# Kernel tuning notes

Measured on AMD Instinct MI355X. Metric: run time of the kernel, lower is better.

Reference implementation:

```python
import jax, jax.numpy as jnp
import numpy as np
from jax import lax

N = 1024          # n_ligand == n_receptor == feature dim (required by broadcast in source)
D = 1024          # gnn_input_dim == gnn_output_dim
H = 32            # hopi_output_dim
C = 32            # cnn_channels


def setup_inputs() -> dict:
    key = jax.random.key(0)
    ks = jax.random.split(key, 24)
    s = 0.02
    inp = {
        "ligand_node_features": jax.random.normal(ks[0], (N, D), jnp.float32),
        "ligand_edge_features": jax.random.normal(ks[1], (N, D), jnp.float32),
        "ligand_adjacency": jax.random.uniform(ks[2], (N, N), jnp.float32),
        "receptor_node_features": jax.random.normal(ks[3], (N, D), jnp.float32),
        "receptor_edge_features": jax.random.normal(ks[4], (N, D), jnp.float32),
        "receptor_adjacency": jax.random.uniform(ks[5], (N, N), jnp.float32),
        # GNNLayer params (shared between ligand and receptor, as in source)
        "Wn": jax.random.normal(ks[6], (D, D), jnp.float32) * s,
        "bn": jax.random.normal(ks[7], (D,), jnp.float32) * s,
        "We": jax.random.normal(ks[8], (D, D), jnp.float32) * s,
        "be": jax.random.normal(ks[9], (D,), jnp.float32) * s,
        "Wa": jax.random.normal(ks[10], (1, D), jnp.float32) * s,
        "ba": jax.random.normal(ks[11], (1,), jnp.float32) * s,
        # HighOrderPairwiseInteraction: Linear(2*D -> H)
        "W_hopi": jax.random.normal(ks[12], (H, 2 * D), jnp.float32) * s,
        "b_hopi": jax.random.normal(ks[13], (H,), jnp.float32) * s,
        # CNN tail
        "conv1_w": jax.random.normal(ks[14], (C, H, 3, 3), jnp.float32) * s,
        "conv1_b": jax.random.normal(ks[15], (C,), jnp.float32) * s,
        "conv2_w": jax.random.normal(ks[16], (C, C, 3, 3), jnp.float32) * s,
        "conv2_b": jax.random.normal(ks[17], (C,), jnp.float32) * s,
        "conv3_w": jax.random.normal(ks[18], (1, C, 1, 1), jnp.float32) * s,
        "conv3_b": jax.random.normal(ks[19], (1,), jnp.float32) * s,
    }
    return inp


def _gnn(nf, ef, Wn, bn, We, be, Wa, ba):
    # aggregated: [N, D]
    agg = jnp.tanh(nf @ Wn.T + bn + ef @ We.T + be)
    scores = agg @ Wa.T + ba                      # [N, 1]
    attn = jax.nn.softmax(scores, axis=1)         # softmax over size-1 dim -> ones (faithful)
    weighted = jnp.sum(agg * attn, axis=1)        # [N]
    return nf + weighted                          # [N,D] + [N] broadcasts over last dim (D == N)


def _conv(x, w, b):
    y = lax.conv_general_dilated(x, w, (1, 1), "SAME",
                                 dimension_numbers=("NCHW", "OIHW", "NCHW"))
    return y + b[None, :, None, None]


def reference(ligand_node_features, ligand_edge_features, ligand_adjacency,
              receptor_node_features, receptor_edge_features, receptor_adjacency,
              Wn, bn, We, be, Wa, ba, W_hopi, b_hopi,
              conv1_w, conv1_b, conv2_w, conv2_b, conv3_w, conv3_b):
    lig = _gnn(ligand_node_features, ligand_edge_features, Wn, bn, We, be, Wa, ba)
    rec = _gnn(receptor_node_features, receptor_edge_features, Wn, bn, We, be, Wa, ba)

    # HOPI: interactions[i, j] = Linear(cat(lig[i], rec[j])) == lig[i] @ Wl.T + rec[j] @ Wr.T + b
    Wl, Wr = W_hopi[:, :D], W_hopi[:, D:]
    lig_p = lig @ Wl.T                            # [N, H]
    rec_p = rec @ Wr.T                            # [N, H]
    interactions = lig_p[:, None, :] + rec_p[None, :, :] + b_hopi  # [N, N, H]

    x = jnp.transpose(interactions, (2, 0, 1))[None]  # [1, H, N, N]
    x = jax.nn.relu(_conv(x, conv1_w, conv1_b))
    x = jax.nn.relu(_conv(x, conv2_w, conv2_b))
    x = _conv(x, conv3_w, conv3_b)                # [1, 1, N, N]
    return x[0, 0]                                # [N, N]
```

## Files before the change

### kernel.cpp

```cpp
#include <hip/hip_runtime.h>


typedef _Float16 half8 __attribute__((ext_vector_type(8)));
typedef _Float16 half4 __attribute__((ext_vector_type(4)));
typedef float    f32x4 __attribute__((ext_vector_type(4)));

__device__ __forceinline__ short f2h_bits(float f){
    _Float16 h = (_Float16)f;
    return __builtin_bit_cast(short, h);
}
__device__ __forceinline__ half8 pack2(const float4& x, const float4& y){
    half8 r;
    r[0] = (_Float16)x.x; r[1] = (_Float16)x.y;
    r[2] = (_Float16)x.z; r[3] = (_Float16)x.w;
    r[4] = (_Float16)y.x; r[5] = (_Float16)y.y;
    r[6] = (_Float16)y.z; r[7] = (_Float16)y.w;
    return r;
}
__device__ __forceinline__ half4 pack4(const float4& x){
    half4 r;
    r[0] = (_Float16)x.x; r[1] = (_Float16)x.y;
    r[2] = (_Float16)x.z; r[3] = (_Float16)x.w;
    return r;
}
__device__ __forceinline__ float tanh_fast(float x){
    float e = __expf(2.f * x);
    return 1.f - 2.f / (e + 1.f);
}

#define SWZ(c) ((((c) >> 1) & 3) << 3)

#define GNN_LOAD(AV, BV, KBN) {                                              \
    const int kbn_ = (KBN) & 2047;                                           \
    const float* Asrc_ = (kbn_ < 1024) ? A0 : A1;                            \
    const float* Bsrc_ = (kbn_ < 1024) ? Wn : We;                            \
    const int kk_ = kbn_ & 1023;                                             \
    const float* ap_ = Asrc_ + (size_t)(j0 + arow) * 1024 + kk_ + akc;       \
    const float* bp_ = Bsrc_ + (size_t)(d0 + brow) * 1024 + kk_ + bkc;       \
    AV[0] = *reinterpret_cast<const float4*>(ap_);                           \
    AV[1] = *reinterpret_cast<const float4*>(ap_ + 4);                       \
    AV[2] = *reinterpret_cast<const float4*>(ap_ + 8);                       \
    AV[3] = *reinterpret_cast<const float4*>(ap_ + 12);                      \
    BV[0] = *reinterpret_cast<const float4*>(bp_);                           \
    BV[1] = *reinterpret_cast<const float4*>(bp_ + 4);                       \
}

#define GNN_STAGE(AV, BV) {                                                  \
    const int ga_ = (t & 3) * 2;                                             \
    const int sa_ = arow & 7;                                                \
    *reinterpret_cast<half8*>(&As[arow * 64 + ((ga_    ) ^ sa_) * 8]) = pack2(AV[0], AV[1]); \
    *reinterpret_cast<half8*>(&As[arow * 64 + ((ga_ + 1) ^ sa_) * 8]) = pack2(AV[2], AV[3]); \
    *reinterpret_cast<half8*>(&Bs[brow * 64 + ((t & 7) ^ (brow & 7)) * 8]) = pack2(BV[0], BV[1]); \
}

#define GNN_MFMA() {                                                         \
    _Pragma("unroll")                                                        \
    for (int ks = 0; ks < 2; ++ks){                                          \
        half8 Af[2], Bf[2];                                                  \
        _Pragma("unroll")                                                    \
        for (int m = 0; m < 2; ++m){                                         \
            int row = wm * 32 + m * 16 + lr;                                 \
            int g   = ((ks * 4 + lg) ^ (row & 7)) * 8;                       \
            Af[m] = *reinterpret_cast<const half8*>(&As[row * 64 + g]);      \
        }                                                                    \
        _Pragma("unroll")                                                    \
        for (int n = 0; n < 2; ++n){                                         \
            int col = wn * 32 + n * 16 + lr;                                 \
            int g   = ((ks * 4 + lg) ^ (col & 7)) * 8;                       \
            Bf[n] = *reinterpret_cast<const half8*>(&Bs[col * 64 + g]);      \
        }                                                                    \
        _Pragma("unroll")                                                    \
        for (int m = 0; m < 2; ++m)                                          \
            _Pragma("unroll")                                                \
            for (int n = 0; n < 2; ++n)                                      \
                acc[m][n] = __builtin_amdgcn_mfma_f32_16x16x32_f16(          \
                    Af[m], Bf[n], acc[m][n], 0, 0, 0);                       \
    }                                                                        \
}

__global__ __launch_bounds__(512) void gnn_kernel(
    const float* __restrict__ lig_nf, const float* __restrict__ lig_ef,
    const float* __restrict__ rec_nf, const float* __restrict__ rec_ef,
    const float* __restrict__ Wn, const float* __restrict__ We,
    const float* __restrict__ bn, const float* __restrict__ be,
    float* __restrict__ part)
{
    __shared__ __attribute__((aligned(16))) short As[128 * 64];
    __shared__ __attribute__((aligned(16))) short Bs[64 * 64];
    __shared__ float red[128][2];

    const int t  = threadIdx.x;
    const int cx = blockIdx.z;
    const float* A0 = cx ? rec_nf : lig_nf;
    const float* A1 = cx ? rec_ef : lig_ef;
    const int j0 = blockIdx.x * 128;
    const int d0 = blockIdx.y * 64;

    const int wid  = t >> 6;
    const int wm   = wid >> 1;
    const int wn   = wid & 1;
    const int lane = t & 63;
    const int lr   = lane & 15;
    const int lg   = lane >> 4;

    f32x4 acc[2][2];
    #pragma unroll
    for (int m = 0; m < 2; ++m)
        #pragma unroll
        for (int n = 0; n < 2; ++n)
            acc[m][n] = (f32x4){0.f, 0.f, 0.f, 0.f};

    const int arow = t >> 2;
    const int akc  = (t & 3) * 16;
    const int brow = t >> 3;
    const int bkc  = (t & 7) * 8;

    float4 avA[4], bvA[2], avB[4], bvB[2];
    GNN_LOAD(avA, bvA, 0);
    GNN_LOAD(avB, bvB, 64);

    for (int kb = 0; kb < 2048; kb += 128){
        __syncthreads();
        GNN_STAGE(avA, bvA);
        GNN_LOAD(avA, bvA, kb + 128);
        __syncthreads();
        GNN_MFMA();
        __syncthreads();
        GNN_STAGE(avB, bvB);
        GNN_LOAD(avB, bvB, kb + 192);
        __syncthreads();
        GNN_MFMA();
    }

    float rowsum[2][4];
    #pragma unroll
    for (int m = 0; m < 2; ++m)
        #pragma unroll
        for (int jj = 0; jj < 4; ++jj) rowsum[m][jj] = 0.f;
    #pragma unroll
    for (int n = 0; n < 2; ++n){
        int d = d0 + wn * 32 + n * 16 + lr;
        float bias = bn[d] + be[d];
        #pragma unroll
        for (int m = 0; m < 2; ++m)
            #pragma unroll
            for (int jj = 0; jj < 4; ++jj)
                rowsum[m][jj] += tanh_fast(acc[m][n][jj] + bias);
    }
    #pragma unroll
    for (int mask = 1; mask < 16; mask <<= 1)
        #pragma unroll
        for (int m = 0; m < 2; ++m)
            #pragma unroll
            for (int jj = 0; jj < 4; ++jj)
                rowsum[m][jj] += __shfl_xor(rowsum[m][jj], mask);
    __syncthreads();
    if (lr == 0){
        #pragma unroll
        for (int m = 0; m < 2; ++m)
            #pragma unroll
            for (int jj = 0; jj < 4; ++jj)
                red[wm * 32 + m * 16 + lg * 4 + jj][wn] = rowsum[m][jj];
    }
    __syncthreads();
    if (t < 128)
        part[(size_t)cx * 16384 + (size_t)blockIdx.y * 1024 + j0 + t]
            = red[t][0] + red[t][1];
}

#define PP_LOAD(AV, BV, KBN) {                                               \
    const int kcol_ = (KBN) & 1023;                                          \
    _Pragma("unroll")                                                        \
    for (int p = 0; p < 3; ++p){                                             \
        int e_ = t + 512 * p;                                                \
        if (e_ < 1280){                                                      \
            int rowl_ = e_ >> 4;                                             \
            int grow_ = r0 - 8 + rowl_;                                      \
            if ((unsigned)grow_ < 1024u)                                     \
                AV[p] = *reinterpret_cast<const float4*>(                    \
                    nf + (size_t)grow_ * 1024 + kcol_ + (e_ & 15) * 4);      \
            else                                                             \
                AV[p] = make_float4(0.f, 0.f, 0.f, 0.f);                     \
        }                                                                    \
    }                                                                        \
    BV = *reinterpret_cast<const float4*>(                                   \
        W + (size_t)(t >> 4) * 2048 + kcol_ + (t & 15) * 4);                 \
}

#define PP_STAGE(AV, BV) {                                                   \
    _Pragma("unroll")                                                        \
    for (int p = 0; p < 3; ++p){                                             \
        int e_ = t + 512 * p;                                                \
        if (e_ < 1280){                                                      \
            int rowl_ = e_ >> 4;                                             \
            int ga_ = (e_ & 15) >> 1;                                        \
            int sub_ = (e_ & 1) * 4;                                         \
            *reinterpret_cast<half4*>(                                       \
                &As[rowl_ * 64 + ((ga_ ^ (rowl_ & 7)) * 8) + sub_]) = pack4(AV[p]); \
        }                                                                    \
    }                                                                        \
    {                                                                        \
        int row_ = t >> 4;                                                   \
        int ga_ = (t & 15) >> 1;                                             \
        int sub_ = (t & 1) * 4;                                              \
        *reinterpret_cast<half4*>(                                           \
            &Bs[row_ * 64 + ((ga_ ^ (row_ & 7)) * 8) + sub_]) = pack4(BV);   \
    }                                                                        \
}

#define PP_MFMA() {                                                          \
    if (wid < 5){                                                            \
        _Pragma("unroll")                                                    \
        for (int ks = 0; ks < 2; ++ks){                                      \
            int ar_ = wid * 16 + lr;                                         \
            half8 Af = *reinterpret_cast<const half8*>(                      \
                &As[ar_ * 64 + ((ks * 4 + lg) ^ (ar_ & 7)) * 8]);            \
            _Pragma("unroll")                                                \
            for (int n = 0; n < 2; ++n){                                     \
                int col_ = n * 16 + lr;                                      \
                half8 Bf = *reinterpret_cast<const half8*>(                  \
                    &Bs[col_ * 64 + ((ks * 4 + lg) ^ (col_ & 7)) * 8]);      \
                pacc[n] = __builtin_amdgcn_mfma_f32_16x16x32_f16(            \
                    Af, Bf, pacc[n], 0, 0, 0);                               \
            }                                                                \
        }                                                                    \
    }                                                                        \
}

__global__ __launch_bounds__(512) void pp_kernel(
    const float* __restrict__ lig_nf, const float* __restrict__ rec_nf,
    const float* __restrict__ W_hopi, const float* __restrict__ b_hopi,
    const float* __restrict__ w1, const float* __restrict__ b1,
    const float* __restrict__ w2,
    const float* __restrict__ part,
    float* __restrict__ Kp, short* __restrict__ U16, short* __restrict__ V16,
    short* __restrict__ w2f16)
{
    __shared__ __attribute__((aligned(16))) char smem[47232];
    const int t = threadIdx.x;
    const int role = blockIdx.x;

    if (role < 32){
        short* As = reinterpret_cast<short*>(smem);
        short* Bs = reinterpret_cast<short*>(smem + 10240);
        short* Pz = reinterpret_cast<short*>(smem + 14336);
        short* Ws = reinterpret_cast<short*>(smem + 20736);

        const int cx = role >> 4;
        const int r0 = (role & 15) * 64;
        const float* nf = cx ? rec_nf : lig_nf;
        const float* W  = W_hopi + (cx ? 1024 : 0);
        short* O = cx ? V16 : U16;

        const int wid = t >> 6;
        const int lane = t & 63;
        const int lr = lane & 15;
        const int lg = lane >> 4;

        for (int e = t; e < 9216; e += 512){
            int cs  = e / 3072;
            int rem = e - cs * 3072;
            int co  = rem / 96;
            int k   = rem - co * 96;
            int d   = k >> 5;
            int ci  = k & 31;
            int o_lo = (cs == 1) ? 1 : 0;
            int o_hi = (cs == 2) ? 1 : 2;
            float s = 0.f;
            for (int o = o_lo; o <= o_hi; ++o){
                int tap = cx ? (o * 3 + d) : (d * 3 + o);
                s += w1[co * 288 + ci * 9 + tap];
            }
            Ws[(cs * 32 + co) * 104 + k] = f2h_bits(s);
        }

        f32x4 pacc[2];
        pacc[0] = (f32x4){0.f, 0.f, 0.f, 0.f};
        pacc[1] = (f32x4){0.f, 0.f, 0.f, 0.f};

        float4 avA[3], avB[3];
        float4 bvA, bvB;
        PP_LOAD(avA, bvA, 0);
        PP_LOAD(avB, bvB, 64);

        for (int kb = 0; kb < 1024; kb += 128){
            __syncthreads();
            PP_STAGE(avA, bvA);
            PP_LOAD(avA, bvA, kb + 128);
            __syncthreads();
            PP_MFMA();
            __syncthreads();
            PP_STAGE(avB, bvB);
            PP_LOAD(avB, bvB, kb + 192);
            __syncthreads();
            PP_MFMA();
        }

        if (wid < 5){
            #pragma unroll
            for (int n = 0; n < 2; ++n)
                #pragma unroll
                for (int jj = 0; jj < 4; ++jj){
                    int rowl = wid * 16 + lg * 4 + jj;
                    Pz[rowl * 40 + n * 16 + lr] = f2h_bits(pacc[n][jj]);
                }
        }
        __syncthreads();

        if (wid < 4){
            f32x4 uacc[3][2];
            #pragma unroll
            for (int cs = 0; cs < 3; ++cs)
                #pragma unroll
                for (int n = 0; n < 2; ++n)
                    uacc[cs][n] = (f32x4){0.f, 0.f, 0.f, 0.f};
            #pragma unroll
            for (int d = 0; d < 3; ++d){
                int ar = wid * 16 + lr;
                half8 Ap = *reinterpret_cast<const half8*>(
                    &Pz[(7 + ar + d) * 40 + lg * 8]);
                #pragma unroll
                for (int cs = 0; cs < 3; ++cs)
                    #pragma unroll
                    for (int n = 0; n < 2; ++n){
                        half8 Bp = *reinterpret_cast<const half8*>(
                            &Ws[(cs * 32 + n * 16 + lr) * 104 + d * 32 + lg * 8]);
                        uacc[cs][n] = __builtin_amdgcn_mfma_f32_16x16x32_f16(
                            Ap, Bp, uacc[cs][n], 0, 0, 0);
                    }
            }
            #pragma unroll
            for (int cs = 0; cs < 3; ++cs)
                #pragma unroll
                for (int n = 0; n < 2; ++n)
                    #pragma unroll
                    for (int jj = 0; jj < 4; ++jj){
                        int grow = r0 + wid * 16 + lg * 4 + jj;
                        O[((size_t)(cs << 10) + grow) * 32 + n * 16 + lr]
                            = f2h_bits(uacc[cs][n][jj]);
                    }
        }
        return;
    }

    if (role == 33){
        for (int e = t; e < 9216; e += 512){
            int co  = e / 288;
            int rem = e - co * 288;
            int ci  = rem / 9;
            int tap = rem - ci * 9;
            w2f16[(tap * 32 + co) * 32 + (ci ^ SWZ(co))] = f2h_bits(w2[e]);
        }
        return;
    }

    float* ws_l = reinterpret_cast<float*>(smem);
    float* ws_r = reinterpret_cast<float*>(smem + 4096);
    float* red  = reinterpret_cast<float*>(smem + 8192);
    float* cvs  = reinterpret_cast<float*>(smem + 10240);
    float* w1s  = reinterpret_cast<float*>(smem + 10368);

    #pragma unroll
    for (int q = 0; q < 5; ++q){
        int i4 = t + q * 512;
        if (i4 < 2304)
            *reinterpret_cast<float4*>(&w1s[i4 * 4]) =
                *reinterpret_cast<const float4*>(w1 + i4 * 4);
    }
    for (int j = t; j < 1024; j += 512){
        float sl = 0.f, sr = 0.f;
        #pragma unroll
        for (int b = 0; b < 16; ++b){
            sl += part[b * 1024 + j];
            sr += part[16384 + b * 1024 + j];
        }
        ws_l[j] = sl; ws_r[j] = sr;
    }
    __syncthreads();
    {
        const int h = t & 31;
        const int seg = t >> 5;
        const float* wl = W_hopi + (size_t)h * 2048 + seg * 64;
        const float* wr = wl + 1024;
        float s = 0.f;
        #pragma unroll 8
        for (int j = 0; j < 64; j += 4){
            float4 a = *reinterpret_cast<const float4*>(wl + j);
            float4 b = *reinterpret_cast<const float4*>(wr + j);
            const float* l = &ws_l[seg * 64 + j];
            const float* r = &ws_r[seg * 64 + j];
            s = fmaf(l[0], a.x, s); s = fmaf(l[1], a.y, s);
            s = fmaf(l[2], a.z, s); s = fmaf(l[3], a.w, s);
            s = fmaf(r[0], b.x, s); s = fmaf(r[1], b.y, s);
            s = fmaf(r[2], b.z, s); s = fmaf(r[3], b.w, s);
        }
        red[t] = s;
    }
    __syncthreads();
    if (t < 32){
        float tot = b_hopi[t];
        #pragma unroll
        for (int g = 0; g < 16; ++g) tot += red[g * 32 + t];
        cvs[t] = tot;
    }
    __syncthreads();
    for (int e = t; e < 288; e += 512){
        int co  = e & 31;
        int cse = e >> 5;
        int yc  = cse / 3, xc = cse - yc * 3;
        float sum = b1[co];
        for (int ci = 0; ci < 32; ++ci){
            const float* wp = &w1s[co * 288 + ci * 9];
            float t00 = wp[0], t01 = wp[1], t02 = wp[2];
            float t10 = wp[3], t11 = wp[4], t12 = wp[5];
            float t20 = wp[6], t21 = wp[7], t22 = wp[8];
            float r0, r1, r2;
            if (xc == 0){ r0 = t00+t01+t02; r1 = t10+t11+t12; r2 = t20+t21+t22; }
            else if (xc == 1){ r0 = t01+t02; r1 = t11+t12; r2 = t21+t22; }
            else { r0 = t00+t01; r1 = t10+t11; r2 = t20+t21; }
            float wsum = (yc == 0) ? (r0+r1+r2) : ((yc == 1) ? (r1+r2) : (r0+r1));
            sum = fmaf(cvs[ci], wsum, sum);
        }
        Kp[cse * 32 + co] = sum;
    }
}

__global__ __launch_bounds__(512) void conv_kernel(
    const short* __restrict__ U16, const short* __restrict__ V16,
    const float* __restrict__ Kp, const short* __restrict__ w2f16,
    const float* __restrict__ b2,
    const float* __restrict__ w3, const float* __restrict__ b3,
    float* __restrict__ outp)
{
    __shared__ __attribute__((aligned(16))) short ys[18 * 18 * 32];
    __shared__ __attribute__((aligned(16))) short wB[9 * 32 * 32];

    const int t    = threadIdx.x;
    const int oy0  = blockIdx.y * 16;
    const int ox0  = blockIdx.x * 16;
    const int wid  = t >> 6;
    const int lane = t & 63;
    const int lr   = lane & 15;
    const int lg   = lane >> 4;

    {
        const uint4* src = reinterpret_cast<const uint4*>(w2f16);
        uint4* dst = reinterpret_cast<uint4*>(wB);
        #pragma unroll
        for (int e = t; e < 1152; e += 512)
            dst[e] = src[e];
    }
    const bool interior = (blockIdx.x >= 1) & (blockIdx.x <= 62) &
                          (blockIdx.y >= 1) & (blockIdx.y <= 62);
    if (interior){
        const int cp = (t & 7) * 4;
        half4 k00;
        {
            float4 kf = *reinterpret_cast<const float4*>(&Kp[cp]);
            k00[0] = (_Float16)kf.x; k00[1] = (_Float16)kf.y;
            k00[2] = (_Float16)kf.z; k00[3] = (_Float16)kf.w;
        }
        #pragma unroll
        for (int pass = 0; pass < 6; ++pass){
            int idx = t + pass * 512;
            if (idx < 2592){
                int po  = idx >> 3;
                int ryo = po / 18;
                int rxo = po - ryo * 18;
                int gy = oy0 - 1 + ryo, gx = ox0 - 1 + rxo;
                half4 u = *reinterpret_cast<const half4*>(&U16[gy * 32 + cp]);
                half4 v = *reinterpret_cast<const half4*>(&V16[gx * 32 + cp]);
                half4 r = u + v + k00;
                #pragma unroll
                for (int e = 0; e < 4; ++e)
                    r[e] = r[e] > (_Float16)0.f ? r[e] : (_Float16)0.f;
                *reinterpret_cast<half4*>(&ys[po * 32 + (cp ^ SWZ(rxo))]) = r;
            }
        }
    } else {
        #pragma unroll
        for (int pass = 0; pass < 6; ++pass){
            int idx = t + pass * 512;
            if (idx < 2592){
                int po  = idx >> 3;
                int cp  = (idx & 7) * 4;
                int ryo = po / 18;
                int rxo = po - ryo * 18;
                int gy = oy0 - 1 + ryo, gx = ox0 - 1 + rxo;
                half4 h = {(_Float16)0.f, (_Float16)0.f, (_Float16)0.f, (_Float16)0.f};
                if ((unsigned)gy < 1024u && (unsigned)gx < 1024u){
                    int yc = (gy == 0) ? 1 : ((gy == 1023) ? 2 : 0);
                    int xc = (gx == 0) ? 1 : ((gx == 1023) ? 2 : 0);
                    half4 u = *reinterpret_cast<const half4*>(
                        &U16[((size_t)(xc << 10) + gy) * 32 + cp]);
                    half4 v = *reinterpret_cast<const half4*>(
                        &V16[((size_t)(yc << 10) + gx) * 32 + cp]);
                    float4 k = *reinterpret_cast<const float4*>(&Kp[(yc * 3 + xc) * 32 + cp]);
                    h[0] = (_Float16)fmaxf((float)u[0] + (float)v[0] + k.x, 0.f);
                    h[1] = (_Float16)fmaxf((float)u[1] + (float)v[1] + k.y, 0.f);
                    h[2] = (_Float16)fmaxf((float)u[2] + (float)v[2] + k.z, 0.f);
                    h[3] = (_Float16)fmaxf((float)u[3] + (float)v[3] + k.w, 0.f);
                }
                *reinterpret_cast<half4*>(&ys[po * 32 + (cp ^ SWZ(rxo))]) = h;
            }
        }
    }
    __syncthreads();

    {
        half8 Bf[2][9];
        float bias[2], w3v[2];
        #pragma unroll
        for (int n = 0; n < 2; ++n){
            int co = n * 16 + lr;
            bias[n] = b2[co];
            w3v[n]  = w3[co];
            #pragma unroll
            for (int tap = 0; tap < 9; ++tap)
                Bf[n][tap] = *reinterpret_cast<const half8*>(
                    &wB[(tap * 32 + co) * 32 + ((lg * 8) ^ SWZ(co))]);
        }
        const float b3v = b3[0];
        for (int s = wid; s < 16; s += 8){
            int p  = s * 16 + lr;
            int ry = p >> 4;
            int rx = p & 15;
            f32x4 acc0 = {0.f, 0.f, 0.f, 0.f};
            f32x4 acc1 = {0.f, 0.f, 0.f, 0.f};
            #pragma unroll
            for (int tap = 0; tap < 9; ++tap){
                const int dy = tap / 3, dx = tap - (tap / 3) * 3;
                int pix = (ry + dy) * 18 + rx + dx;
                half8 A = *reinterpret_cast<const half8*>(
                    &ys[pix * 32 + ((lg * 8) ^ SWZ(rx + dx))]);
                acc0 = __builtin_amdgcn_mfma_f32_16x16x32_f16(A, Bf[0][tap], acc0, 0, 0, 0);
                acc1 = __builtin_amdgcn_mfma_f32_16x16x32_f16(A, Bf[1][tap], acc1, 0, 0, 0);
            }
            float part[4];
            #pragma unroll
            for (int j = 0; j < 4; ++j)
                part[j] = w3v[0] * fmaxf(acc0[j] + bias[0], 0.f)
                        + w3v[1] * fmaxf(acc1[j] + bias[1], 0.f);
            #pragma unroll
            for (int m = 1; m < 16; m <<= 1)
                #pragma unroll
                for (int j = 0; j < 4; ++j)
                    part[j] += __shfl_xor(part[j], m);
            if (lr == 0){
                float4 o = make_float4(part[0] + b3v, part[1] + b3v,
                                       part[2] + b3v, part[3] + b3v);
                *reinterpret_cast<float4*>(outp + (size_t)(oy0 + s) * 1024 + ox0 + lg * 4) = o;
            }
        }
    }
}

extern "C" void kernel_launch(void* const* d_in, const int* in_sizes, int n_in,
                              void* d_out, int out_size, void* d_ws, size_t ws_size,
                              hipStream_t stream)
{
    const float* lig_nf = (const float*)d_in[0];
    const float* lig_ef = (const float*)d_in[1];
    const float* rec_nf = (const float*)d_in[3];
    const float* rec_ef = (const float*)d_in[4];
    const float* Wn     = (const float*)d_in[6];
    const float* bn     = (const float*)d_in[7];
    const float* We     = (const float*)d_in[8];
    const float* be     = (const float*)d_in[9];
    const float* W_hopi = (const float*)d_in[12];
    const float* b_hopi = (const float*)d_in[13];
    const float* w1     = (const float*)d_in[14];
    const float* b1     = (const float*)d_in[15];
    const float* w2     = (const float*)d_in[16];
    const float* b2     = (const float*)d_in[17];
    const float* w3     = (const float*)d_in[18];
    const float* b3     = (const float*)d_in[19];
    float* outp = (float*)d_out;

    float* part  = (float*)d_ws;
    float* Kp    = (float*)((char*)d_ws + 393216);
    short* U16   = (short*)((char*)d_ws + 394368);
    short* V16   = (short*)((char*)d_ws + 590976);
    short* w2f16 = (short*)((char*)d_ws + 787584);

    dim3 g1(8, 16, 2);
    gnn_kernel<<<g1, 512, 0, stream>>>(lig_nf, lig_ef, rec_nf, rec_ef,
                                       Wn, We, bn, be, part);
    pp_kernel<<<34, 512, 0, stream>>>(lig_nf, rec_nf, W_hopi, b_hopi,
                                      w1, b1, w2, part, Kp, U16, V16, w2f16);
    dim3 g3(64, 64);
    conv_kernel<<<g3, 512, 0, stream>>>(U16, V16, Kp, w2f16, b2, w3, b3, outp);
}
```

Baseline: 114.9 us.

## Make conv blocks persistent over 8 tiles with double-buffered LDS and prefetch

The conv kernel now launches 512 blocks, each handling 8 horizontally adjacent 16x16 output tiles. The U rows and the conv2 weight fragments are loaded once and reused across those tiles, and the next tile's V values are prefetched into registers while MFMA work runs on a double-buffered LDS tile. The build also uses 8-wide half vectors instead of 4-wide, and the weight-prep loops in pp_kernel are unrolled. This cuts the per-block setup cost and the global loads, at the price of fewer concurrent blocks (512 on 256 CUs), more LDS and more registers per block.

```diff
diff --git a/kernel.cpp b/kernel.cpp
--- a/kernel.cpp
+++ b/kernel.cpp
@@ -257,7 +257,9 @@
         const int lr = lane & 15;
         const int lg = lane >> 4;
 
-        for (int e = t; e < 9216; e += 512){
+        #pragma unroll
+        for (int q = 0; q < 18; ++q){
+            int e = t + q * 512;
             int cs  = e / 3072;
             int rem = e - cs * 3072;
             int co  = rem / 96;
@@ -344,7 +346,9 @@
     }
 
     if (role == 33){
-        for (int e = t; e < 9216; e += 512){
+        #pragma unroll
+        for (int q = 0; q < 18; ++q){
+            int e = t + q * 512;
             int co  = e / 288;
             int rem = e - co * 288;
             int ci  = rem / 9;
@@ -432,17 +436,20 @@
     const float* __restrict__ w3, const float* __restrict__ b3,
     float* __restrict__ outp)
 {
-    __shared__ __attribute__((aligned(16))) short ys[18 * 18 * 32];
+    __shared__ __attribute__((aligned(16))) short ysbuf[2][18 * 18 * 32];
     __shared__ __attribute__((aligned(16))) short wB[9 * 32 * 32];
 
     const int t    = threadIdx.x;
-    const int oy0  = blockIdx.y * 16;
-    const int ox0  = blockIdx.x * 16;
     const int wid  = t >> 6;
     const int lane = t & 63;
     const int lr   = lane & 15;
     const int lg   = lane >> 4;
 
+    const int ty  = blockIdx.x >> 3;
+    const int oy0 = ty * 16;
+    const int tx0 = (blockIdx.x & 7) * 8;
+    const bool rowInt = (ty >= 1) && (ty <= 62);
+
     {
         const uint4* src = reinterpret_cast<const uint4*>(w2f16);
         uint4* dst = reinterpret_cast<uint4*>(wB);
@@ -450,81 +457,114 @@
         for (int e = t; e < 1152; e += 512)
             dst[e] = src[e];
     }
-    const bool interior = (blockIdx.x >= 1) & (blockIdx.x <= 62) &
-                          (blockIdx.y >= 1) & (blockIdx.y <= 62);
-    if (interior){
-        const int cp = (t & 7) * 4;
-        half4 k00;
-        {
-            float4 kf = *reinterpret_cast<const float4*>(&Kp[cp]);
-            k00[0] = (_Float16)kf.x; k00[1] = (_Float16)kf.y;
-            k00[2] = (_Float16)kf.z; k00[3] = (_Float16)kf.w;
-        }
-        #pragma unroll
-        for (int pass = 0; pass < 6; ++pass){
-            int idx = t + pass * 512;
-            if (idx < 2592){
-                int po  = idx >> 3;
-                int ryo = po / 18;
-                int rxo = po - ryo * 18;
-                int gy = oy0 - 1 + ryo, gx = ox0 - 1 + rxo;
-                half4 u = *reinterpret_cast<const half4*>(&U16[gy * 32 + cp]);
-                half4 v = *reinterpret_cast<const half4*>(&V16[gx * 32 + cp]);
-                half4 r = u + v + k00;
-                #pragma unroll
-                for (int e = 0; e < 4; ++e)
+
+    const int c8 = (t & 3) * 8;
+    int poA[3], ryoA[3], rxoA[3];
+    bool act[3];
+    #pragma unroll
+    for (int p = 0; p < 3; ++p){
+        int idx = t + p * 512;
+        act[p] = idx < 1296;
+        int po = act[p] ? (idx >> 2) : 0;
+        poA[p]  = po;
+        ryoA[p] = po / 18;
+        rxoA[p] = po - ryoA[p] * 18;
+    }
+
+    half8 k00;
+    {
+        float4 ka = *reinterpret_cast<const float4*>(&Kp[c8]);
+        float4 kb = *reinterpret_cast<const float4*>(&Kp[c8 + 4]);
+        k00 = pack2(ka, kb);
+    }
+
+    half8 uq[3];
+    if (rowInt){
+        #pragma unroll
+        for (int p = 0; p < 3; ++p)
+            if (act[p])
+                uq[p] = *reinterpret_cast<const half8*>(
+                    &U16[(oy0 - 1 + ryoA[p]) * 32 + c8]);
+    }
+    half8 vq[3];
+    if (rowInt && tx0 >= 1){
+        #pragma unroll
+        for (int p = 0; p < 3; ++p)
+            if (act[p])
+                vq[p] = *reinterpret_cast<const half8*>(
+                    &V16[(tx0 * 16 - 1 + rxoA[p]) * 32 + c8]);
+    }
+    __syncthreads();
+
+    half8 Bf[2][9];
+    float bias[2], w3v[2];
+    #pragma unroll
+    for (int n = 0; n < 2; ++n){
+        int co = n * 16 + lr;
+        bias[n] = b2[co];
+        w3v[n]  = w3[co];
+        #pragma unroll
+        for (int tap = 0; tap < 9; ++tap)
+            Bf[n][tap] = *reinterpret_cast<const half8*>(
+                &wB[(tap * 32 + co) * 32 + ((lg * 8) ^ SWZ(co))]);
+    }
+    const float b3v = b3[0];
+
+    int cur = 0;
+    for (int i = 0; i < 8; ++i){
+        const int tx  = tx0 + i;
+        const int ox0 = tx * 16;
+        const bool fast = rowInt && (tx >= 1) && (tx <= 62);
+        short* ys = ysbuf[cur];
+
+        if (fast){
+            #pragma unroll
+            for (int p = 0; p < 3; ++p) if (act[p]){
+                half8 r = uq[p] + vq[p] + k00;
+                #pragma unroll
+                for (int e = 0; e < 8; ++e)
                     r[e] = r[e] > (_Float16)0.f ? r[e] : (_Float16)0.f;
-                *reinterpret_cast<half4*>(&ys[po * 32 + (cp ^ SWZ(rxo))]) = r;
+                *reinterpret_cast<half8*>(&ys[poA[p] * 32 + (c8 ^ SWZ(rxoA[p]))]) = r;
             }
-        }
-    } else {
-        #pragma unroll
-        for (int pass = 0; pass < 6; ++pass){
-            int idx = t + pass * 512;
-            if (idx < 2592){
-                int po  = idx >> 3;
-                int cp  = (idx & 7) * 4;
-                int ryo = po / 18;
-                int rxo = po - ryo * 18;
-                int gy = oy0 - 1 + ryo, gx = ox0 - 1 + rxo;
-                half4 h = {(_Float16)0.f, (_Float16)0.f, (_Float16)0.f, (_Float16)0.f};
+        } else {
+            #pragma unroll
+            for (int p = 0; p < 3; ++p) if (act[p]){
+                int gy = oy0 - 1 + ryoA[p];
+                int gx = ox0 - 1 + rxoA[p];
+                half8 h;
+                #pragma unroll
+                for (int e = 0; e < 8; ++e) h[e] = (_Float16)0.f;
                 if ((unsigned)gy < 1024u && (unsigned)gx < 1024u){
                     int yc = (gy == 0) ? 1 : ((gy == 1023) ? 2 : 0);
                     int xc = (gx == 0) ? 1 : ((gx == 1023) ? 2 : 0);
-                    half4 u = *reinterpret_cast<const half4*>(
-                        &U16[((size_t)(xc << 10) + gy) * 32 + cp]);
-                    half4 v = *reinterpret_cast<const half4*>(
-                        &V16[((size_t)(yc << 10) + gx) * 32 + cp]);
-                    float4 k = *reinterpret_cast<const float4*>(&Kp[(yc * 3 + xc) * 32 + cp]);
-                    h[0] = (_Float16)fmaxf((float)u[0] + (float)v[0] + k.x, 0.f);
-                    h[1] = (_Float16)fmaxf((float)u[1] + (float)v[1] + k.y, 0.f);
-                    h[2] = (_Float16)fmaxf((float)u[2] + (float)v[2] + k.z, 0.f);
-                    h[3] = (_Float16)fmaxf((float)u[3] + (float)v[3] + k.w, 0.f);
+                    half8 u = *reinterpret_cast<const half8*>(
+                        &U16[((size_t)(xc << 10) + gy) * 32 + c8]);
+                    half8 v = *reinterpret_cast<const half8*>(
+                        &V16[((size_t)(yc << 10) + gx) * 32 + c8]);
+                    const float* kp = &Kp[(yc * 3 + xc) * 32 + c8];
+                    #pragma unroll
+                    for (int e = 0; e < 8; ++e)
+                        h[e] = (_Float16)fmaxf((float)u[e] + (float)v[e] + kp[e], 0.f);
                 }
-                *reinterpret_cast<half4*>(&ys[po * 32 + (cp ^ SWZ(rxo))]) = h;
+                *reinterpret_cast<half8*>(&ys[poA[p] * 32 + (c8 ^ SWZ(rxoA[p]))]) = h;
             }
         }
-    }
-    __syncthreads();
-
-    {
-        half8 Bf[2][9];
-        float bias[2], w3v[2];
-        #pragma unroll
-        for (int n = 0; n < 2; ++n){
-            int co = n * 16 + lr;
-            bias[n] = b2[co];
-            w3v[n]  = w3[co];
-            #pragma unroll
-            for (int tap = 0; tap < 9; ++tap)
-                Bf[n][tap] = *reinterpret_cast<const half8*>(
-                    &wB[(tap * 32 + co) * 32 + ((lg * 8) ^ SWZ(co))]);
-        }
-        const float b3v = b3[0];
+        __syncthreads();
+
+        if (i < 7){
+            const int txn = tx + 1;
+            if (rowInt && txn >= 1 && txn <= 62){
+                #pragma unroll
+                for (int p = 0; p < 3; ++p)
+                    if (act[p])
+                        vq[p] = *reinterpret_cast<const half8*>(
+                            &V16[(txn * 16 - 1 + rxoA[p]) * 32 + c8]);
+            }
+        }
+
         for (int s = wid; s < 16; s += 8){
-            int p  = s * 16 + lr;
-            int ry = p >> 4;
-            int rx = p & 15;
+            const int ry = s;
+            const int rx = lr;
             f32x4 acc0 = {0.f, 0.f, 0.f, 0.f};
             f32x4 acc1 = {0.f, 0.f, 0.f, 0.f};
             #pragma unroll
@@ -552,6 +592,7 @@
                 *reinterpret_cast<float4*>(outp + (size_t)(oy0 + s) * 1024 + ox0 + lg * 4) = o;
             }
         }
+        cur ^= 1;
     }
 }
 
@@ -588,6 +629,5 @@
                                        Wn, We, bn, be, part);
     pp_kernel<<<34, 512, 0, stream>>>(lig_nf, rec_nf, W_hopi, b_hopi,
                                       w1, b1, w2, part, Kp, U16, V16, w2f16);
-    dim3 g3(64, 64);
-    conv_kernel<<<g3, 512, 0, stream>>>(U16, V16, Kp, w2f16, b2, w3, b3, outp);
-}
+    conv_kernel<<<512, 512, 0, stream>>>(U16, V16, Kp, w2f16, b2, w3, b3, outp);
+}
```

Result: no change. 116.8 us (+1.7%).
